# Kernel tuning notes

Measured on AMD Instinct MI355X. Metric: run time of the kernel, lower is better.

The kernel has to match this reference:

```python
import jax, jax.numpy as jnp
import numpy as np

N_NODES = 50000
N_EDGES = 1600000
IN_C = 256
HID_C = 128
OUT_C = 16
HEADS = 8
NEG_SLOPE = 0.2  # PyG GATConv default


def gat_layer(x, src, dst, W, att_src, att_dst, bias, heads, out_c):
    """PyG-style GATConv (eval mode, add_self_loops already applied to src/dst).
    x: [N, F_in], W: [F_in, heads*out_c], att_*: [heads, out_c], bias: [heads*out_c].
    Returns concatenated heads: [N, heads*out_c]."""
    N = x.shape[0]
    h = (x @ W).reshape(N, heads, out_c)                  # [N, H, C]
    a_src = (h * att_src[None]).sum(-1)                   # [N, H]
    a_dst = (h * att_dst[None]).sum(-1)                   # [N, H]
    alpha = a_src[src] + a_dst[dst]                       # [E, H]
    alpha = jax.nn.leaky_relu(alpha, NEG_SLOPE)
    # segment softmax over incoming edges of each destination node
    amax = jax.ops.segment_max(alpha, dst, num_segments=N)  # [N, H]
    alpha = jnp.exp(alpha - jax.lax.stop_gradient(amax)[dst])
    denom = jax.ops.segment_sum(alpha, dst, num_segments=N)  # [N, H]
    w = alpha / denom[dst]                                # [E, H]
    msg = h[src] * w[:, :, None]                          # [E, H, C]
    out = jax.ops.segment_sum(msg, dst, num_segments=N)   # [N, H, C]
    return out.reshape(N, heads * out_c) + bias


def setup_inputs() -> dict:
    key = jax.random.key(0)
    ks = jax.random.split(key, 10)
    x = jax.random.normal(ks[0], (N_NODES, IN_C), dtype=jnp.float32)
    edge_index = jax.random.randint(ks[1], (2, N_EDGES), 0, N_NODES, dtype=jnp.int32)
    c1 = HID_C // HEADS  # 16 per head
    s1 = 1.0 / np.sqrt(IN_C)
    s2 = 1.0 / np.sqrt(HID_C)
    return {
        "x": x,
        "edge_index": edge_index,
        "W1": jax.random.normal(ks[2], (IN_C, HEADS * c1), dtype=jnp.float32) * s1,
        "att_src1": jax.random.normal(ks[3], (HEADS, c1), dtype=jnp.float32) * s1,
        "att_dst1": jax.random.normal(ks[4], (HEADS, c1), dtype=jnp.float32) * s1,
        "bias1": jnp.zeros((HEADS * c1,), dtype=jnp.float32),
        "W2": jax.random.normal(ks[5], (HID_C, OUT_C), dtype=jnp.float32) * s2,
        "att_src2": jax.random.normal(ks[6], (1, OUT_C), dtype=jnp.float32) * s2,
        "att_dst2": jax.random.normal(ks[7], (1, OUT_C), dtype=jnp.float32) * s2,
        "bias2": jnp.zeros((OUT_C,), dtype=jnp.float32),
    }


def reference(x, edge_index, W1, att_src1, att_dst1, bias1, W2, att_src2, att_dst2, bias2):
    N = x.shape[0]
    loop = jnp.arange(N, dtype=edge_index.dtype)
    src = jnp.concatenate([edge_index[0], loop])  # add_self_loops=True (PyG default)
    dst = jnp.concatenate([edge_index[1], loop])
    h = gat_layer(x, src, dst, W1, att_src1, att_dst1, bias1, HEADS, HID_C // HEADS)
    h = jax.nn.relu(h)
    # F.dropout with training=False is identity (eval mode)
    out = gat_layer(h, src, dst, W2, att_src2, att_dst2, bias2, 1, OUT_C)
    return out
```

## Files before the change

### kernel.cpp

```cpp
#include <hip/hip_runtime.h>
#include <hip/hip_bf16.h>


#define NN 50000
#define NE 1600000
#define NBK 196
#define NB_SC 512
#define CHUNK (NE / NB_SC)
#define NCH (NB_SC * 4)

typedef __attribute__((ext_vector_type(8))) short bf16x8;
typedef __attribute__((ext_vector_type(4))) float f32x4;

__device__ __forceinline__ float lrelu(float x) { return fmaxf(x, 0.2f * x); }

__device__ __forceinline__ float ldf(const void* p, int i, int isbf) {
  return isbf ? __bfloat162float(((const __hip_bfloat16*)p)[i])
              : ((const float*)p)[i];
}
__device__ __forceinline__ short f2bf_bits(float v) {
  __hip_bfloat16 h = __float2bfloat16(v);
  return *reinterpret_cast<short*>(&h);
}
__device__ __forceinline__ float bfs2f(short b) {
  unsigned int u = ((unsigned int)(unsigned short)b) << 16;
  union { unsigned int u; float f; } c; c.u = u; return c.f;
}

#define OFF_H1   ((size_t)0)
#define OFF_H    ((size_t)25600000)
#define OFF_H2   ((size_t)51200000)
#define OFF_AS1  ((size_t)54400000)
#define OFF_AD1  ((size_t)56000000)
#define OFF_AS2  ((size_t)57600000)
#define OFF_AD2  ((size_t)57800000)
#define OFF_CNT  ((size_t)58000000)
#define OFF_OFFS ((size_t)58400000)
#define OFF_CSR  ((size_t)58600000)
#define OFF_WP1  ((size_t)65000000)
#define OFF_BCNT ((size_t)65065536)
#define OFF_BBASE ((size_t)65066560)
#define OFF_FLAG ((size_t)65068608)

__global__ void detect_dtype(const unsigned int* __restrict__ x, int* __restrict__ flag) {
  __shared__ int s[256];
  int t = threadIdx.x;
  unsigned int w = x[t * 97 + 5];
  unsigned int e = (w >> 7) & 0xFF;
  s[t] = (e >= 116 && e <= 138) ? 1 : 0;
  __syncthreads();
  for (int off = 128; off > 0; off >>= 1) {
    if (t < off) s[t] += s[t + off];
    __syncthreads();
  }
  if (t == 0) *flag = (s[0] >= 128) ? 1 : 0;
}

__global__ void repack_w1(const void* __restrict__ W1, short* __restrict__ Wp,
                          const int* __restrict__ flag) {
  int i = blockIdx.x * 256 + threadIdx.x;
  if (i >= 256 * 128) return;
  int f = *flag;
  int j = i & 7, q = (i >> 3) & 3, c = (i >> 5) & 127, t = i >> 12;
  int src = (t * 32 + q * 8 + j) * 128 + c;
  Wp[i] = f ? ((const short*)W1)[src] : f2bf_bits(((const float*)W1)[src]);
}

__global__ __launch_bounds__(256) void gemm1(const void* __restrict__ X,
                                             const short* __restrict__ Wp,
                                             short* __restrict__ H1b,
                                             const int* __restrict__ flag) {
  int wave = threadIdx.x >> 6, lane = threadIdx.x & 63;
  int rowbase = blockIdx.x * 64 + wave * 16;
  int l15 = lane & 15, quad = lane >> 4;
  int f = *flag;
  int arow = rowbase + l15;
  if (arow >= NN) arow = NN - 1;
  f32x4 acc[8];
#pragma unroll
  for (int ct = 0; ct < 8; ++ct) acc[ct] = (f32x4){0.f, 0.f, 0.f, 0.f};
  size_t abase = (size_t)arow * 256 + quad * 8;
#pragma unroll
  for (int kt = 0; kt < 8; ++kt) {
    bf16x8 a;
    if (f) {
      a = *(const bf16x8*)((const short*)X + abase + kt * 32);
    } else {
      const float* xp = (const float*)X + abase + kt * 32;
      float4 v0 = *(const float4*)xp, v1 = *(const float4*)(xp + 4);
      a[0] = f2bf_bits(v0.x); a[1] = f2bf_bits(v0.y);
      a[2] = f2bf_bits(v0.z); a[3] = f2bf_bits(v0.w);
      a[4] = f2bf_bits(v1.x); a[5] = f2bf_bits(v1.y);
      a[6] = f2bf_bits(v1.z); a[7] = f2bf_bits(v1.w);
    }
#pragma unroll
    for (int ct = 0; ct < 8; ++ct) {
      bf16x8 b = *(const bf16x8*)(Wp + ((kt * 128 + ct * 16 + l15) * 4 + quad) * 8);
      acc[ct] = __builtin_amdgcn_mfma_f32_16x16x32_bf16(a, b, acc[ct], 0, 0, 0);
    }
  }
  int r0 = rowbase + quad * 4;
#pragma unroll
  for (int ct = 0; ct < 8; ++ct)
#pragma unroll
    for (int r = 0; r < 4; ++r) {
      int row = r0 + r;
      if (row < NN) H1b[(size_t)row * 128 + ct * 16 + l15] = f2bf_bits(acc[ct][r]);
    }
}

__global__ void calc_a1(const short* __restrict__ H1b, const void* __restrict__ as1,
                        const void* __restrict__ ad1, float* __restrict__ AS,
                        float* __restrict__ AD, const int* __restrict__ flag) {
  __shared__ float s_as[128], s_ad[128];
  int t = threadIdx.x;
  int f = *flag;
  if (t < 128) { s_as[t] = ldf(as1, t, f); s_ad[t] = ldf(ad1, t, f); }
  __syncthreads();
  int tid = blockIdx.x * 256 + t;
  if (tid >= NN * 8) return;
  int n = tid >> 3, hh = tid & 7;
  const bf16x8* hp = (const bf16x8*)(H1b + (size_t)n * 128 + hh * 16);
  bf16x8 v0 = hp[0], v1 = hp[1];
  float as = 0.f, ad = 0.f;
#pragma unroll
  for (int i = 0; i < 8; ++i) {
    int b = hh * 16 + i;
    float x0 = bfs2f(v0[i]), x1 = bfs2f(v1[i]);
    as += x0 * s_as[b] + x1 * s_as[b + 8];
    ad += x0 * s_ad[b] + x1 * s_ad[b + 8];
  }
  AS[tid] = as; AD[tid] = ad;
}

__global__ __launch_bounds__(256) void scat_hist(const int* __restrict__ dst,
                                                 int* __restrict__ HB) {
  __shared__ int h[4][224];
  int t = threadIdx.x, w = t >> 6;
  for (int i = t; i < 4 * 224; i += 256) (&h[0][0])[i] = 0;
  __syncthreads();
  int e0 = blockIdx.x * CHUNK, e1 = e0 + CHUNK;
  for (int e = e0 + t; e < e1; e += 256) atomicAdd(&h[w][dst[e] >> 8], 1);
  __syncthreads();
  int chunk0 = blockIdx.x * 4;
  for (int i = t; i < 4 * NBK; i += 256) {
    int ww = i / NBK, k = i - ww * NBK;
    HB[(chunk0 + ww) * NBK + k] = h[ww][k];
  }
}

__global__ __launch_bounds__(256) void scat_scan1(int* __restrict__ HB,
                                                  int* __restrict__ total) {
  __shared__ int ts[256];
  int k = blockIdx.x, t = threadIdx.x;
  int base = t * 8;
  int v[8]; int s = 0;
#pragma unroll
  for (int i = 0; i < 8; ++i) { v[i] = HB[(base + i) * NBK + k]; s += v[i]; }
  ts[t] = s;
  __syncthreads();
  for (int off = 1; off < 256; off <<= 1) {
    int a = (t >= off) ? ts[t - off] : 0;
    __syncthreads();
    ts[t] += a;
    __syncthreads();
  }
  int ex = ts[t] - s;
#pragma unroll
  for (int i = 0; i < 8; ++i) { HB[(base + i) * NBK + k] = ex; ex += v[i]; }
  if (t == 255) total[k] = ts[255];
}

__global__ void scat_scan2(const int* __restrict__ total, int* __restrict__ bbase,
                           int* __restrict__ bcnt) {
  __shared__ int sd[256];
  int t = threadIdx.x;
  int v = (t < NBK) ? total[t] : 0;
  sd[t] = v;
  __syncthreads();
  for (int off = 1; off < 256; off <<= 1) {
    int a = (t >= off) ? sd[t - off] : 0;
    __syncthreads();
    sd[t] += a;
    __syncthreads();
  }
  if (t < NBK) { bbase[t] = sd[t] - v; bcnt[t] = v; }
}

__global__ __launch_bounds__(256) void scat_write(const int* __restrict__ src,
                                                  const int* __restrict__ dst,
                                                  const int* __restrict__ HB,
                                                  const int* __restrict__ bbase,
                                                  int2* __restrict__ EP) {
  __shared__ int sc[4][224];
  int t = threadIdx.x, w = t >> 6, lane = t & 63;
  int chunk = blockIdx.x * 4 + w;
  for (int k = lane; k < NBK; k += 64)
    sc[w][k] = bbase[k] + HB[chunk * NBK + k];
  __syncthreads();
  int e0 = blockIdx.x * CHUNK, e1 = e0 + CHUNK;
  for (int e = e0 + t; e < e1; e += 256) {
    int d = dst[e];
    int p = atomicAdd(&sc[w][d >> 8], 1);
    EP[p] = make_int2(src[e], d);
  }
}

__global__ __launch_bounds__(256) void bucket_csr(const int2* __restrict__ EP,
                                                  const int* __restrict__ bcnt,
                                                  const int* __restrict__ bbase,
                                                  int* __restrict__ cnt,
                                                  int* __restrict__ offs,
                                                  int* __restrict__ csr) {
  __shared__ int h[256], sc[256], lc[256];
  int b = blockIdx.x, t = threadIdx.x;
  int gbase = bbase[b], n = bcnt[b];
  h[t] = 0;
  __syncthreads();
  for (int i = t; i < n; i += 256) atomicAdd(&h[EP[gbase + i].y & 255], 1);
  __syncthreads();
  int v = h[t];
  sc[t] = v;
  __syncthreads();
  for (int off = 1; off < 256; off <<= 1) {
    int add = (t >= off) ? sc[t - off] : 0;
    __syncthreads();
    sc[t] += add;
    __syncthreads();
  }
  int ex = sc[t] - v;
  int node = (b << 8) + t;
  if (node < NN) { cnt[node] = v; offs[node] = gbase + ex; }
  lc[t] = ex;
  __syncthreads();
  for (int i = t; i < n; i += 256) {
    int2 p = EP[gbase + i];
    int pos = atomicAdd(&lc[p.y & 255], 1);
    csr[gbase + pos] = p.x;
  }
}

__global__ __launch_bounds__(256) void agg1(const short* __restrict__ H1b,
                                            const float* __restrict__ AS,
                                            const float* __restrict__ AD,
                                            const int* __restrict__ offs,
                                            const int* __restrict__ cnt,
                                            const int* __restrict__ csr,
                                            const void* __restrict__ bias1,
                                            short* __restrict__ Hb,
                                            const int* __restrict__ flag) {
  int lane = threadIdx.x & 63;
  int node = blockIdx.x * 4 + (threadIdx.x >> 6);
  int f = *flag;
  int start = offs[node], deg = cnt[node];
  int g = lane >> 3, k = lane & 7;
  float adst = AD[node * 8 + k];
  float acc[16];
#pragma unroll
  for (int i = 0; i < 16; ++i) acc[i] = 0.f;
  float dsum = 0.f;
  if (g == 0) {
    float p = __expf(lrelu(AS[node * 8 + k] + adst));
    dsum = p;
    const bf16x8* hp = (const bf16x8*)(H1b + (size_t)node * 128 + k * 16);
    bf16x8 v0 = hp[0], v1 = hp[1];
#pragma unroll
    for (int i = 0; i < 8; ++i) {
      acc[i] = p * bfs2f(v0[i]);
      acc[8 + i] = p * bfs2f(v1[i]);
    }
  }
  int s = (g < deg) ? csr[start + g] : -1;
  for (int eb = 0; eb < deg; eb += 8) {
    int en = eb + 8 + g;
    int sn = (en < deg) ? csr[start + en] : -1;
    if (s >= 0) {
      float p = __expf(lrelu(AS[s * 8 + k] + adst));
      const bf16x8* hp = (const bf16x8*)(H1b + (size_t)s * 128 + k * 16);
      bf16x8 v0 = hp[0], v1 = hp[1];
      dsum += p;
#pragma unroll
      for (int i = 0; i < 8; ++i) {
        acc[i] += p * bfs2f(v0[i]);
        acc[8 + i] += p * bfs2f(v1[i]);
      }
    }
    s = sn;
  }
#pragma unroll
  for (int i = 0; i < 16; ++i) {
    acc[i] += __shfl_xor(acc[i], 8);
    acc[i] += __shfl_xor(acc[i], 16);
    acc[i] += __shfl_xor(acc[i], 32);
  }
  dsum += __shfl_xor(dsum, 8);
  dsum += __shfl_xor(dsum, 16);
  dsum += __shfl_xor(dsum, 32);
  if (g == 0) {
    float inv = 1.0f / dsum;
    int c0 = k * 16;
    bf16x8 o0, o1;
#pragma unroll
    for (int i = 0; i < 8; ++i) {
      o0[i] = f2bf_bits(fmaxf(acc[i] * inv + ldf(bias1, c0 + i, f), 0.f));
      o1[i] = f2bf_bits(fmaxf(acc[8 + i] * inv + ldf(bias1, c0 + 8 + i, f), 0.f));
    }
    *(bf16x8*)(Hb + (size_t)node * 128 + c0) = o0;
    *(bf16x8*)(Hb + (size_t)node * 128 + c0 + 8) = o1;
  }
}

__global__ __launch_bounds__(256) void gemm2_a2(const short* __restrict__ Hb,
                                                const void* __restrict__ W2,
                                                const void* __restrict__ as2,
                                                const void* __restrict__ ad2,
                                                float* __restrict__ H2,
                                                float* __restrict__ AS2,
                                                float* __restrict__ AD2,
                                                const int* __restrict__ flag) {
  __shared__ float sW[2048];
  __shared__ float s_as[16], s_ad[16];
  int t = threadIdx.x;
  int f = *flag;
  for (int i = t; i < 2048; i += 256) sW[i] = ldf(W2, i, f);
  if (t < 16) { s_as[t] = ldf(as2, t, f); s_ad[t] = ldf(ad2, t, f); }
  __syncthreads();
  int n = blockIdx.x * 16 + (t >> 4), c = t & 15;
  const bf16x8* hp = (const bf16x8*)(Hb + (size_t)n * 128);
  float acc = 0.f;
#pragma unroll 4
  for (int k8 = 0; k8 < 16; ++k8) {
    bf16x8 v = hp[k8];
#pragma unroll
    for (int i = 0; i < 8; ++i) acc += bfs2f(v[i]) * sW[(k8 * 8 + i) * 16 + c];
  }
  H2[n * 16 + c] = acc;
  float vs = acc * s_as[c], vd = acc * s_ad[c];
#pragma unroll
  for (int off = 1; off < 16; off <<= 1) {
    vs += __shfl_xor(vs, off);
    vd += __shfl_xor(vd, off);
  }
  if (c == 0) { AS2[n] = vs; AD2[n] = vd; }
}

__global__ __launch_bounds__(256) void agg2(const float* __restrict__ H2,
                                            const float* __restrict__ AS2,
                                            const float* __restrict__ AD2,
                                            const int* __restrict__ offs,
                                            const int* __restrict__ cnt,
                                            const int* __restrict__ csr,
                                            const void* __restrict__ bias2,
                                            void* __restrict__ outv,
                                            const int* __restrict__ flag) {
  int lane = threadIdx.x & 63;
  int node = blockIdx.x * 4 + (threadIdx.x >> 6);
  int f = *flag;
  int start = offs[node], deg = cnt[node];
  int g = lane >> 3, k = lane & 7;
  float adst = AD2[node];
  float a0 = 0.f, a1 = 0.f, dsum = 0.f;
  if (g == 0) {
    float p = __expf(lrelu(AS2[node] + adst));
    dsum = p;
    float2 v = *(const float2*)(H2 + (size_t)node * 16 + k * 2);
    a0 = p * v.x; a1 = p * v.y;
  }
  int s = (g < deg) ? csr[start + g] : -1;
  for (int eb = 0; eb < deg; eb += 8) {
    int en = eb + 8 + g;
    int sn = (en < deg) ? csr[start + en] : -1;
    if (s >= 0) {
      float p = __expf(lrelu(AS2[s] + adst));
      float2 v = *(const float2*)(H2 + (size_t)s * 16 + k * 2);
      dsum += p;
      a0 += p * v.x; a1 += p * v.y;
    }
    s = sn;
  }
  a0 += __shfl_xor(a0, 8);  a0 += __shfl_xor(a0, 16);  a0 += __shfl_xor(a0, 32);
  a1 += __shfl_xor(a1, 8);  a1 += __shfl_xor(a1, 16);  a1 += __shfl_xor(a1, 32);
  dsum += __shfl_xor(dsum, 8); dsum += __shfl_xor(dsum, 16); dsum += __shfl_xor(dsum, 32);
  if (g == 0) {
    float inv = 1.0f / dsum;
    float o0 = a0 * inv + ldf(bias2, k * 2 + 0, f);
    float o1 = a1 * inv + ldf(bias2, k * 2 + 1, f);
    size_t base = (size_t)node * 16 + k * 2;
    if (f) {
      ((__hip_bfloat16*)outv)[base] = __float2bfloat16(o0);
      ((__hip_bfloat16*)outv)[base + 1] = __float2bfloat16(o1);
    } else {
      *(float2*)((float*)outv + base) = make_float2(o0, o1);
    }
  }
}

extern "C" void kernel_launch(void* const* d_in, const int* in_sizes, int n_in,
                              void* d_out, int out_size, void* d_ws, size_t ws_size,
                              hipStream_t stream) {
  const void* x = d_in[0];
  const int* ei = (const int*)d_in[1];
  const void* W1 = d_in[2];
  const void* as1 = d_in[3];
  const void* ad1 = d_in[4];
  const void* b1 = d_in[5];
  const void* W2 = d_in[6];
  const void* as2 = d_in[7];
  const void* ad2 = d_in[8];
  const void* b2 = d_in[9];
  char* ws = (char*)d_ws;

  short* H1b = (short*)(ws + OFF_H1);
  short* Hb = (short*)(ws + OFF_H);
  int2* EP = (int2*)(ws + OFF_H);
  float* H2 = (float*)(ws + OFF_H2);
  int* HB = (int*)(ws + OFF_H2);
  float* AS1 = (float*)(ws + OFF_AS1);
  float* AD1 = (float*)(ws + OFF_AD1);
  float* AS2 = (float*)(ws + OFF_AS2);
  float* AD2 = (float*)(ws + OFF_AD2);
  int* CNT = (int*)(ws + OFF_CNT);
  int* OFFS = (int*)(ws + OFF_OFFS);
  int* CSR = (int*)(ws + OFF_CSR);
  short* Wp = (short*)(ws + OFF_WP1);
  int* BCNT = (int*)(ws + OFF_BCNT);
  int* BBASE = (int*)(ws + OFF_BBASE);
  int* FLAG = (int*)(ws + OFF_FLAG);

  detect_dtype<<<1, 256, 0, stream>>>((const unsigned int*)x, FLAG);
  repack_w1<<<128, 256, 0, stream>>>(W1, Wp, FLAG);
  gemm1<<<(NN + 63) / 64, 256, 0, stream>>>(x, Wp, H1b, FLAG);
  calc_a1<<<(NN * 8 + 255) / 256, 256, 0, stream>>>(H1b, as1, ad1, AS1, AD1, FLAG);

  scat_hist<<<NB_SC, 256, 0, stream>>>(ei + NE, HB);
  scat_scan1<<<NBK, 256, 0, stream>>>(HB, BCNT);
  scat_scan2<<<1, 256, 0, stream>>>(BCNT, BBASE, BCNT);
  scat_write<<<NB_SC, 256, 0, stream>>>(ei, ei + NE, HB, BBASE, EP);
  bucket_csr<<<NBK, 256, 0, stream>>>(EP, BCNT, BBASE, CNT, OFFS, CSR);

  agg1<<<NN / 4, 256, 0, stream>>>(H1b, AS1, AD1, OFFS, CNT, CSR, b1, Hb, FLAG);
  gemm2_a2<<<NN / 16, 256, 0, stream>>>(Hb, W2, as2, ad2, H2, AS2, AD2, FLAG);
  agg2<<<NN / 4, 256, 0, stream>>>(H2, AS2, AD2, OFFS, CNT, CSR, b2, d_out, FLAG);
}
```

Before: 312.0 us.

## Merge independent kernels, compress edge and CSR indices, prefetch neighbors, store H2 fp16

Merges gemm1 with the destination histogram and calc_a1 with the per-bucket scan into two block-partitioned launches, so independent work shares a grid and two launches disappear. Packs scattered edges into 32-bit words (local dst byte plus 16-bit src), stores the CSR as 16-bit indices and runs bucket_csr with 1024 threads, which cuts index traffic. agg1 and agg2 now prefetch the next neighbor's attention score and features one iteration ahead. H2 is stored in fp16 to halve layer-2 gather bytes. The 16-bit indices rely on the node count staying below 65536, and fp16 H2 adds some rounding error.

```diff
diff --git a/kernel.cpp b/kernel.cpp
--- a/kernel.cpp
+++ b/kernel.cpp
@@ -8,6 +8,8 @@
 #define NB_SC 512
 #define CHUNK (NE / NB_SC)
 #define NCH (NB_SC * 4)
+#define GB1 782
+#define GB2 1563
 
 typedef __attribute__((ext_vector_type(8))) short bf16x8;
 typedef __attribute__((ext_vector_type(4))) float f32x4;
@@ -25,6 +27,14 @@
 __device__ __forceinline__ float bfs2f(short b) {
   unsigned int u = ((unsigned int)(unsigned short)b) << 16;
   union { unsigned int u; float f; } c; c.u = u; return c.f;
+}
+__device__ __forceinline__ unsigned short f2h_bits(float v) {
+  _Float16 h = (_Float16)v;
+  return *reinterpret_cast<unsigned short*>(&h);
+}
+__device__ __forceinline__ float h2f(unsigned short b) {
+  _Float16 h = *reinterpret_cast<_Float16*>(&b);
+  return (float)h;
 }
 
 #define OFF_H1   ((size_t)0)
@@ -66,109 +76,115 @@
   Wp[i] = f ? ((const short*)W1)[src] : f2bf_bits(((const float*)W1)[src]);
 }
 
-__global__ __launch_bounds__(256) void gemm1(const void* __restrict__ X,
-                                             const short* __restrict__ Wp,
-                                             short* __restrict__ H1b,
-                                             const int* __restrict__ flag) {
-  int wave = threadIdx.x >> 6, lane = threadIdx.x & 63;
-  int rowbase = blockIdx.x * 64 + wave * 16;
-  int l15 = lane & 15, quad = lane >> 4;
-  int f = *flag;
-  int arow = rowbase + l15;
-  if (arow >= NN) arow = NN - 1;
-  f32x4 acc[8];
-#pragma unroll
-  for (int ct = 0; ct < 8; ++ct) acc[ct] = (f32x4){0.f, 0.f, 0.f, 0.f};
-  size_t abase = (size_t)arow * 256 + quad * 8;
-#pragma unroll
-  for (int kt = 0; kt < 8; ++kt) {
-    bf16x8 a;
-    if (f) {
-      a = *(const bf16x8*)((const short*)X + abase + kt * 32);
-    } else {
-      const float* xp = (const float*)X + abase + kt * 32;
-      float4 v0 = *(const float4*)xp, v1 = *(const float4*)(xp + 4);
-      a[0] = f2bf_bits(v0.x); a[1] = f2bf_bits(v0.y);
-      a[2] = f2bf_bits(v0.z); a[3] = f2bf_bits(v0.w);
-      a[4] = f2bf_bits(v1.x); a[5] = f2bf_bits(v1.y);
-      a[6] = f2bf_bits(v1.z); a[7] = f2bf_bits(v1.w);
-    }
-#pragma unroll
-    for (int ct = 0; ct < 8; ++ct) {
-      bf16x8 b = *(const bf16x8*)(Wp + ((kt * 128 + ct * 16 + l15) * 4 + quad) * 8);
-      acc[ct] = __builtin_amdgcn_mfma_f32_16x16x32_bf16(a, b, acc[ct], 0, 0, 0);
-    }
-  }
-  int r0 = rowbase + quad * 4;
-#pragma unroll
-  for (int ct = 0; ct < 8; ++ct)
-#pragma unroll
-    for (int r = 0; r < 4; ++r) {
-      int row = r0 + r;
-      if (row < NN) H1b[(size_t)row * 128 + ct * 16 + l15] = f2bf_bits(acc[ct][r]);
-    }
-}
-
-__global__ void calc_a1(const short* __restrict__ H1b, const void* __restrict__ as1,
-                        const void* __restrict__ ad1, float* __restrict__ AS,
-                        float* __restrict__ AD, const int* __restrict__ flag) {
+__global__ __launch_bounds__(256) void fat1(const void* __restrict__ X,
+                                            const short* __restrict__ Wp,
+                                            short* __restrict__ H1b,
+                                            const int* __restrict__ flag,
+                                            const int* __restrict__ dst,
+                                            int* __restrict__ HB) {
+  __shared__ int h[4][224];
+  if (blockIdx.x < GB1) {
+    int wave = threadIdx.x >> 6, lane = threadIdx.x & 63;
+    int rowbase = blockIdx.x * 64 + wave * 16;
+    int l15 = lane & 15, quad = lane >> 4;
+    int f = *flag;
+    int arow = rowbase + l15;
+    if (arow >= NN) arow = NN - 1;
+    f32x4 acc[8];
+#pragma unroll
+    for (int ct = 0; ct < 8; ++ct) acc[ct] = (f32x4){0.f, 0.f, 0.f, 0.f};
+    size_t abase = (size_t)arow * 256 + quad * 8;
+#pragma unroll
+    for (int kt = 0; kt < 8; ++kt) {
+      bf16x8 a;
+      if (f) {
+        a = *(const bf16x8*)((const short*)X + abase + kt * 32);
+      } else {
+        const float* xp = (const float*)X + abase + kt * 32;
+        float4 v0 = *(const float4*)xp, v1 = *(const float4*)(xp + 4);
+        a[0] = f2bf_bits(v0.x); a[1] = f2bf_bits(v0.y);
+        a[2] = f2bf_bits(v0.z); a[3] = f2bf_bits(v0.w);
+        a[4] = f2bf_bits(v1.x); a[5] = f2bf_bits(v1.y);
+        a[6] = f2bf_bits(v1.z); a[7] = f2bf_bits(v1.w);
+      }
+#pragma unroll
+      for (int ct = 0; ct < 8; ++ct) {
+        bf16x8 b = *(const bf16x8*)(Wp + ((kt * 128 + ct * 16 + l15) * 4 + quad) * 8);
+        acc[ct] = __builtin_amdgcn_mfma_f32_16x16x32_bf16(a, b, acc[ct], 0, 0, 0);
+      }
+    }
+    int r0 = rowbase + quad * 4;
+#pragma unroll
+    for (int ct = 0; ct < 8; ++ct)
+#pragma unroll
+      for (int r = 0; r < 4; ++r) {
+        int row = r0 + r;
+        if (row < NN) H1b[(size_t)row * 128 + ct * 16 + l15] = f2bf_bits(acc[ct][r]);
+      }
+  } else {
+    int b = blockIdx.x - GB1;
+    int t = threadIdx.x, w = t >> 6;
+    for (int i = t; i < 4 * 224; i += 256) (&h[0][0])[i] = 0;
+    __syncthreads();
+    int e0 = b * CHUNK, e1 = e0 + CHUNK;
+    for (int e = e0 + t; e < e1; e += 256) atomicAdd(&h[w][dst[e] >> 8], 1);
+    __syncthreads();
+    int chunk0 = b * 4;
+    for (int i = t; i < 4 * NBK; i += 256) {
+      int ww = i / NBK, k = i - ww * NBK;
+      HB[(chunk0 + ww) * NBK + k] = h[ww][k];
+    }
+  }
+}
+
+__global__ __launch_bounds__(256) void fat2(const short* __restrict__ H1b,
+                                            const void* __restrict__ as1,
+                                            const void* __restrict__ ad1,
+                                            float* __restrict__ AS,
+                                            float* __restrict__ AD,
+                                            const int* __restrict__ flag,
+                                            int* __restrict__ HB,
+                                            int* __restrict__ total) {
   __shared__ float s_as[128], s_ad[128];
+  __shared__ int ts[256];
   int t = threadIdx.x;
-  int f = *flag;
-  if (t < 128) { s_as[t] = ldf(as1, t, f); s_ad[t] = ldf(ad1, t, f); }
-  __syncthreads();
-  int tid = blockIdx.x * 256 + t;
-  if (tid >= NN * 8) return;
-  int n = tid >> 3, hh = tid & 7;
-  const bf16x8* hp = (const bf16x8*)(H1b + (size_t)n * 128 + hh * 16);
-  bf16x8 v0 = hp[0], v1 = hp[1];
-  float as = 0.f, ad = 0.f;
-#pragma unroll
-  for (int i = 0; i < 8; ++i) {
-    int b = hh * 16 + i;
-    float x0 = bfs2f(v0[i]), x1 = bfs2f(v1[i]);
-    as += x0 * s_as[b] + x1 * s_as[b + 8];
-    ad += x0 * s_ad[b] + x1 * s_ad[b + 8];
-  }
-  AS[tid] = as; AD[tid] = ad;
-}
-
-__global__ __launch_bounds__(256) void scat_hist(const int* __restrict__ dst,
-                                                 int* __restrict__ HB) {
-  __shared__ int h[4][224];
-  int t = threadIdx.x, w = t >> 6;
-  for (int i = t; i < 4 * 224; i += 256) (&h[0][0])[i] = 0;
-  __syncthreads();
-  int e0 = blockIdx.x * CHUNK, e1 = e0 + CHUNK;
-  for (int e = e0 + t; e < e1; e += 256) atomicAdd(&h[w][dst[e] >> 8], 1);
-  __syncthreads();
-  int chunk0 = blockIdx.x * 4;
-  for (int i = t; i < 4 * NBK; i += 256) {
-    int ww = i / NBK, k = i - ww * NBK;
-    HB[(chunk0 + ww) * NBK + k] = h[ww][k];
-  }
-}
-
-__global__ __launch_bounds__(256) void scat_scan1(int* __restrict__ HB,
-                                                  int* __restrict__ total) {
-  __shared__ int ts[256];
-  int k = blockIdx.x, t = threadIdx.x;
-  int base = t * 8;
-  int v[8]; int s = 0;
-#pragma unroll
-  for (int i = 0; i < 8; ++i) { v[i] = HB[(base + i) * NBK + k]; s += v[i]; }
-  ts[t] = s;
-  __syncthreads();
-  for (int off = 1; off < 256; off <<= 1) {
-    int a = (t >= off) ? ts[t - off] : 0;
-    __syncthreads();
-    ts[t] += a;
-    __syncthreads();
-  }
-  int ex = ts[t] - s;
-#pragma unroll
-  for (int i = 0; i < 8; ++i) { HB[(base + i) * NBK + k] = ex; ex += v[i]; }
-  if (t == 255) total[k] = ts[255];
+  if (blockIdx.x < GB2) {
+    int f = *flag;
+    if (t < 128) { s_as[t] = ldf(as1, t, f); s_ad[t] = ldf(ad1, t, f); }
+    __syncthreads();
+    int tid = blockIdx.x * 256 + t;
+    if (tid >= NN * 8) return;
+    int n = tid >> 3, hh = tid & 7;
+    const bf16x8* hp = (const bf16x8*)(H1b + (size_t)n * 128 + hh * 16);
+    bf16x8 v0 = hp[0], v1 = hp[1];
+    float as = 0.f, ad = 0.f;
+#pragma unroll
+    for (int i = 0; i < 8; ++i) {
+      int b = hh * 16 + i;
+      float x0 = bfs2f(v0[i]), x1 = bfs2f(v1[i]);
+      as += x0 * s_as[b] + x1 * s_as[b + 8];
+      ad += x0 * s_ad[b] + x1 * s_ad[b + 8];
+    }
+    AS[tid] = as; AD[tid] = ad;
+  } else {
+    int k = blockIdx.x - GB2;
+    int base = t * 8;
+    int v[8]; int s = 0;
+#pragma unroll
+    for (int i = 0; i < 8; ++i) { v[i] = HB[(base + i) * NBK + k]; s += v[i]; }
+    ts[t] = s;
+    __syncthreads();
+    for (int off = 1; off < 256; off <<= 1) {
+      int a = (t >= off) ? ts[t - off] : 0;
+      __syncthreads();
+      ts[t] += a;
+      __syncthreads();
+    }
+    int ex = ts[t] - s;
+#pragma unroll
+    for (int i = 0; i < 8; ++i) { HB[(base + i) * NBK + k] = ex; ex += v[i]; }
+    if (t == 255) total[k] = ts[255];
+  }
 }
 
 __global__ void scat_scan2(const int* __restrict__ total, int* __restrict__ bbase,
@@ -191,7 +207,7 @@
                                                   const int* __restrict__ dst,
                                                   const int* __restrict__ HB,
                                                   const int* __restrict__ bbase,
-                                                  int2* __restrict__ EP) {
+                                                  unsigned int* __restrict__ EPp) {
   __shared__ int sc[4][224];
   int t = threadIdx.x, w = t >> 6, lane = t & 63;
   int chunk = blockIdx.x * 4 + w;
@@ -202,41 +218,43 @@
   for (int e = e0 + t; e < e1; e += 256) {
     int d = dst[e];
     int p = atomicAdd(&sc[w][d >> 8], 1);
-    EP[p] = make_int2(src[e], d);
-  }
-}
-
-__global__ __launch_bounds__(256) void bucket_csr(const int2* __restrict__ EP,
-                                                  const int* __restrict__ bcnt,
-                                                  const int* __restrict__ bbase,
-                                                  int* __restrict__ cnt,
-                                                  int* __restrict__ offs,
-                                                  int* __restrict__ csr) {
+    EPp[p] = ((unsigned int)(d & 255) << 16) | (unsigned int)src[e];
+  }
+}
+
+__global__ __launch_bounds__(1024) void bucket_csr(const unsigned int* __restrict__ EPp,
+                                                   const int* __restrict__ bcnt,
+                                                   const int* __restrict__ bbase,
+                                                   int* __restrict__ cnt,
+                                                   int* __restrict__ offs,
+                                                   unsigned short* __restrict__ csr) {
   __shared__ int h[256], sc[256], lc[256];
   int b = blockIdx.x, t = threadIdx.x;
   int gbase = bbase[b], n = bcnt[b];
-  h[t] = 0;
-  __syncthreads();
-  for (int i = t; i < n; i += 256) atomicAdd(&h[EP[gbase + i].y & 255], 1);
-  __syncthreads();
-  int v = h[t];
-  sc[t] = v;
+  if (t < 256) h[t] = 0;
+  __syncthreads();
+  for (int i = t; i < n; i += 1024) atomicAdd(&h[(EPp[gbase + i] >> 16) & 255], 1);
+  __syncthreads();
+  int v = 0;
+  if (t < 256) { v = h[t]; sc[t] = v; }
   __syncthreads();
   for (int off = 1; off < 256; off <<= 1) {
-    int add = (t >= off) ? sc[t - off] : 0;
-    __syncthreads();
-    sc[t] += add;
-    __syncthreads();
-  }
-  int ex = sc[t] - v;
-  int node = (b << 8) + t;
-  if (node < NN) { cnt[node] = v; offs[node] = gbase + ex; }
-  lc[t] = ex;
-  __syncthreads();
-  for (int i = t; i < n; i += 256) {
-    int2 p = EP[gbase + i];
-    int pos = atomicAdd(&lc[p.y & 255], 1);
-    csr[gbase + pos] = p.x;
+    int add = (t >= off && t < 256) ? sc[t - off] : 0;
+    __syncthreads();
+    if (t < 256) sc[t] += add;
+    __syncthreads();
+  }
+  if (t < 256) {
+    int ex = sc[t] - v;
+    int node = (b << 8) + t;
+    if (node < NN) { cnt[node] = v; offs[node] = gbase + ex; }
+    lc[t] = ex;
+  }
+  __syncthreads();
+  for (int i = t; i < n; i += 1024) {
+    unsigned int p = EPp[gbase + i];
+    int pos = atomicAdd(&lc[(p >> 16) & 255], 1);
+    csr[gbase + pos] = (unsigned short)(p & 0xFFFF);
   }
 }
 
@@ -245,7 +263,7 @@
                                             const float* __restrict__ AD,
                                             const int* __restrict__ offs,
                                             const int* __restrict__ cnt,
-                                            const int* __restrict__ csr,
+                                            const unsigned short* __restrict__ csr,
                                             const void* __restrict__ bias1,
                                             short* __restrict__ Hb,
                                             const int* __restrict__ flag) {
@@ -270,14 +288,24 @@
       acc[8 + i] = p * bfs2f(v1[i]);
     }
   }
-  int s = (g < deg) ? csr[start + g] : -1;
+  int s = (g < deg) ? (int)csr[start + g] : -1;
+  float a_c = 0.f; bf16x8 v0, v1;
+  if (s >= 0) {
+    a_c = AS[s * 8 + k];
+    const bf16x8* hp = (const bf16x8*)(H1b + (size_t)s * 128 + k * 16);
+    v0 = hp[0]; v1 = hp[1];
+  }
   for (int eb = 0; eb < deg; eb += 8) {
     int en = eb + 8 + g;
-    int sn = (en < deg) ? csr[start + en] : -1;
+    int sn = (en < deg) ? (int)csr[start + en] : -1;
+    float a_n = 0.f; bf16x8 w0, w1;
+    if (sn >= 0) {
+      a_n = AS[sn * 8 + k];
+      const bf16x8* hp = (const bf16x8*)(H1b + (size_t)sn * 128 + k * 16);
+      w0 = hp[0]; w1 = hp[1];
+    }
     if (s >= 0) {
-      float p = __expf(lrelu(AS[s * 8 + k] + adst));
-      const bf16x8* hp = (const bf16x8*)(H1b + (size_t)s * 128 + k * 16);
-      bf16x8 v0 = hp[0], v1 = hp[1];
+      float p = __expf(lrelu(a_c + adst));
       dsum += p;
 #pragma unroll
       for (int i = 0; i < 8; ++i) {
@@ -285,7 +313,7 @@
         acc[8 + i] += p * bfs2f(v1[i]);
       }
     }
-    s = sn;
+    s = sn; a_c = a_n; v0 = w0; v1 = w1;
   }
 #pragma unroll
   for (int i = 0; i < 16; ++i) {
@@ -314,7 +342,7 @@
                                                 const void* __restrict__ W2,
                                                 const void* __restrict__ as2,
                                                 const void* __restrict__ ad2,
-                                                float* __restrict__ H2,
+                                                unsigned short* __restrict__ H2h,
                                                 float* __restrict__ AS2,
                                                 float* __restrict__ AD2,
                                                 const int* __restrict__ flag) {
@@ -334,7 +362,7 @@
 #pragma unroll
     for (int i = 0; i < 8; ++i) acc += bfs2f(v[i]) * sW[(k8 * 8 + i) * 16 + c];
   }
-  H2[n * 16 + c] = acc;
+  H2h[n * 16 + c] = f2h_bits(acc);
   float vs = acc * s_as[c], vd = acc * s_ad[c];
 #pragma unroll
   for (int off = 1; off < 16; off <<= 1) {
@@ -344,12 +372,12 @@
   if (c == 0) { AS2[n] = vs; AD2[n] = vd; }
 }
 
-__global__ __launch_bounds__(256) void agg2(const float* __restrict__ H2,
+__global__ __launch_bounds__(256) void agg2(const unsigned short* __restrict__ H2h,
                                             const float* __restrict__ AS2,
                                             const float* __restrict__ AD2,
                                             const int* __restrict__ offs,
                                             const int* __restrict__ cnt,
-                                            const int* __restrict__ csr,
+                                            const unsigned short* __restrict__ csr,
                                             const void* __restrict__ bias2,
                                             void* __restrict__ outv,
                                             const int* __restrict__ flag) {
@@ -363,20 +391,31 @@
   if (g == 0) {
     float p = __expf(lrelu(AS2[node] + adst));
     dsum = p;
-    float2 v = *(const float2*)(H2 + (size_t)node * 16 + k * 2);
-    a0 = p * v.x; a1 = p * v.y;
-  }
-  int s = (g < deg) ? csr[start + g] : -1;
+    unsigned int hv = *(const unsigned int*)(H2h + (size_t)node * 16 + k * 2);
+    a0 = p * h2f((unsigned short)(hv & 0xFFFF));
+    a1 = p * h2f((unsigned short)(hv >> 16));
+  }
+  int s = (g < deg) ? (int)csr[start + g] : -1;
+  float as_c = 0.f; unsigned int hv_c = 0;
+  if (s >= 0) {
+    as_c = AS2[s];
+    hv_c = *(const unsigned int*)(H2h + (size_t)s * 16 + k * 2);
+  }
   for (int eb = 0; eb < deg; eb += 8) {
     int en = eb + 8 + g;
-    int sn = (en < deg) ? csr[start + en] : -1;
+    int sn = (en < deg) ? (int)csr[start + en] : -1;
+    float as_n = 0.f; unsigned int hv_n = 0;
+    if (sn >= 0) {
+      as_n = AS2[sn];
+      hv_n = *(const unsigned int*)(H2h + (size_t)sn * 16 + k * 2);
+    }
     if (s >= 0) {
-      float p = __expf(lrelu(AS2[s] + adst));
-      float2 v = *(const float2*)(H2 + (size_t)s * 16 + k * 2);
+      float p = __expf(lrelu(as_c + adst));
       dsum += p;
-      a0 += p * v.x; a1 += p * v.y;
-    }
-    s = sn;
+      a0 += p * h2f((unsigned short)(hv_c & 0xFFFF));
+      a1 += p * h2f((unsigned short)(hv_c >> 16));
+    }
+    s = sn; as_c = as_n; hv_c = hv_n;
   }
   a0 += __shfl_xor(a0, 8);  a0 += __shfl_xor(a0, 16);  a0 += __shfl_xor(a0, 32);
   a1 += __shfl_xor(a1, 8);  a1 += __shfl_xor(a1, 16);  a1 += __shfl_xor(a1, 32);
@@ -412,8 +451,8 @@
 
   short* H1b = (short*)(ws + OFF_H1);
   short* Hb = (short*)(ws + OFF_H);
-  int2* EP = (int2*)(ws + OFF_H);
-  float* H2 = (float*)(ws + OFF_H2);
+  unsigned int* EPp = (unsigned int*)(ws + OFF_H);
+  unsigned short* H2h = (unsigned short*)(ws + OFF_H2);
   int* HB = (int*)(ws + OFF_H2);
   float* AS1 = (float*)(ws + OFF_AS1);
   float* AD1 = (float*)(ws + OFF_AD1);
@@ -421,7 +460,7 @@
   float* AD2 = (float*)(ws + OFF_AD2);
   int* CNT = (int*)(ws + OFF_CNT);
   int* OFFS = (int*)(ws + OFF_OFFS);
-  int* CSR = (int*)(ws + OFF_CSR);
+  unsigned short* CSR = (unsigned short*)(ws + OFF_CSR);
   short* Wp = (short*)(ws + OFF_WP1);
   int* BCNT = (int*)(ws + OFF_BCNT);
   int* BBASE = (int*)(ws + OFF_BBASE);
@@ -429,16 +468,13 @@
 
   detect_dtype<<<1, 256, 0, stream>>>((const unsigned int*)x, FLAG);
   repack_w1<<<128, 256, 0, stream>>>(W1, Wp, FLAG);
-  gemm1<<<(NN + 63) / 64, 256, 0, stream>>>(x, Wp, H1b, FLAG);
-  calc_a1<<<(NN * 8 + 255) / 256, 256, 0, stream>>>(H1b, as1, ad1, AS1, AD1, FLAG);
-
-  scat_hist<<<NB_SC, 256, 0, stream>>>(ei + NE, HB);
-  scat_scan1<<<NBK, 256, 0, stream>>>(HB, BCNT);
+  fat1<<<GB1 + NB_SC, 256, 0, stream>>>(x, Wp, H1b, FLAG, ei + NE, HB);
+  fat2<<<GB2 + NBK, 256, 0, stream>>>(H1b, as1, ad1, AS1, AD1, FLAG, HB, BCNT);
   scat_scan2<<<1, 256, 0, stream>>>(BCNT, BBASE, BCNT);
-  scat_write<<<NB_SC, 256, 0, stream>>>(ei, ei + NE, HB, BBASE, EP);
-  bucket_csr<<<NBK, 256, 0, stream>>>(EP, BCNT, BBASE, CNT, OFFS, CSR);
+  scat_write<<<NB_SC, 256, 0, stream>>>(ei, ei + NE, HB, BBASE, EPp);
+  bucket_csr<<<NBK, 1024, 0, stream>>>(EPp, BCNT, BBASE, CNT, OFFS, CSR);
 
   agg1<<<NN / 4, 256, 0, stream>>>(H1b, AS1, AD1, OFFS, CNT, CSR, b1, Hb, FLAG);
-  gemm2_a2<<<NN / 16, 256, 0, stream>>>(Hb, W2, as2, ad2, H2, AS2, AD2, FLAG);
-  agg2<<<NN / 4, 256, 0, stream>>>(H2, AS2, AD2, OFFS, CNT, CSR, b2, d_out, FLAG);
-}
+  gemm2_a2<<<NN / 16, 256, 0, stream>>>(Hb, W2, as2, ad2, H2h, AS2, AD2, FLAG);
+  agg2<<<NN / 4, 256, 0, stream>>>(H2h, AS2, AD2, OFFS, CNT, CSR, b2, d_out, FLAG);
+}
```

New measurement: 275.3 us. 1.13x faster.
